# Optimization experiments

Measured on AMD Instinct MI355X. Metric: run time of the kernel, lower is better.

## Reference

```python
import jax, jax.numpy as jnp
import numpy as np

K = 3  # neighbors for knn_interpolate


def _knn_interpolate(x, pos, pos_skip, B, k):
    """PyG knn_interpolate with equal-sized batches.
    x: [N_coarse, C], pos: [N_coarse, 3], pos_skip: [N_fine, 3].
    """
    C = x.shape[1]
    xb = x.reshape(B, -1, C)          # [B, nc, C]
    pb = pos.reshape(B, -1, 3)        # [B, nc, 3]
    qb = pos_skip.reshape(B, -1, 3)   # [B, nf, 3]

    def per_cloud(xf, pf, qf):
        # squared distances [nf, nc]
        d2 = jnp.sum((qf[:, None, :] - pf[None, :, :]) ** 2, axis=-1)
        neg_d2k, idx = jax.lax.top_k(-d2, k)          # k smallest distances
        d2k = -neg_d2k                                # [nf, k]
        w = 1.0 / jnp.clip(d2k, 1e-16)                # inverse-distance weights
        w = jax.lax.stop_gradient(w)                  # PyG computes weights under no_grad
        feats = xf[idx]                               # [nf, k, C] gather
        return jnp.sum(w[..., None] * feats, axis=1) / jnp.sum(w, axis=1, keepdims=True)

    y = jax.vmap(per_cloud)(xb, pb, qb)               # [B, nf, C]
    return y.reshape(-1, C)


def setup_inputs() -> dict:
    key = jax.random.key(0)
    ks = jax.random.split(key, 8)
    B, n_coarse, n_fine = 16, 1024, 4096
    C_in, C_skip, C_mid, C_out = 256, 128, 256, 256
    x = jax.random.normal(ks[0], (B * n_coarse, C_in), jnp.float32)
    pos = jax.random.uniform(ks[1], (B * n_coarse, 3), jnp.float32)
    x_skip = jax.random.normal(ks[2], (B * n_fine, C_skip), jnp.float32)
    pos_skip = jax.random.uniform(ks[3], (B * n_fine, 3), jnp.float32)
    batch = jnp.repeat(jnp.arange(B, dtype=jnp.int64), n_coarse)
    batch_skip = jnp.repeat(jnp.arange(B, dtype=jnp.int64), n_fine)
    seed_idx = jnp.arange(B * n_coarse, dtype=jnp.int64)
    seed_idx_skip = jnp.arange(B * n_fine, dtype=jnp.int64)
    W1 = jax.random.normal(ks[4], (C_in + C_skip, C_mid), jnp.float32) * 0.05
    b1 = jnp.zeros((C_mid,), jnp.float32)
    W2 = jax.random.normal(ks[5], (C_mid, C_out), jnp.float32) * 0.05
    b2 = jnp.zeros((C_out,), jnp.float32)
    return {"x": x, "pos": pos, "batch": batch, "seed_idx": seed_idx,
            "x_skip": x_skip, "pos_skip": pos_skip, "batch_skip": batch_skip,
            "seed_idx_skip": seed_idx_skip, "W1": W1, "b1": b1, "W2": W2, "b2": b2}


def reference(x, pos, batch, seed_idx, x_skip, pos_skip, batch_skip, seed_idx_skip,
              W1, b1, W2, b2):
    B = int(batch[-1]) + 1  # equal-sized contiguous clouds
    y = _knn_interpolate(x, pos, pos_skip, B, K)      # [N_fine, C_in]
    h = jnp.concatenate([y, x_skip], axis=1)          # [N_fine, C_in+C_skip]
    h = jax.nn.relu(h @ W1 + b1)                      # MLP layer 1
    out = jax.nn.relu(h @ W2 + b2)                    # MLP layer 2
    return (out, pos_skip, batch_skip)
```

## Files before the change

kernel.cpp:

```cpp
#include <hip/hip_runtime.h>
#include <hip/hip_bf16.h>

#define NB    16
#define NC    1024
#define NF    4096
#define NFINE (NB*NF)
#define CIN   256
#define CSKIP 128
#define KH    (CIN+CSKIP)
#define CMID  256
#define COUT  256

typedef __attribute__((ext_vector_type(8))) short short8;
typedef __attribute__((ext_vector_type(4))) float f32x4;
typedef __attribute__((ext_vector_type(4))) unsigned int u32x4;

__device__ __forceinline__ float bf2f(short s) {
    return __uint_as_float(((unsigned)(unsigned short)s) << 16);
}

__global__ __launch_bounds__(256)
void binprep_kernel(const float* __restrict__ pos,
                    float* __restrict__ gp, int* __restrict__ gcs,
                    const float* __restrict__ W1, const float* __restrict__ W2,
                    __hip_bfloat16* __restrict__ W1at,
                    __hip_bfloat16* __restrict__ imgG,
                    __hip_bfloat16* __restrict__ img2)
{
    __shared__ int cnt[512];
    __shared__ float lx[NC], ly[NC], lz[NC];
    __shared__ short lcell[NC];
    const int t = threadIdx.x;
    if (blockIdx.x >= NB) {
        int e = (blockIdx.x - NB)*256 + t;
        if (e < CMID*CIN) {
            int n = e / CIN, k = e % CIN;
            W1at[e] = __float2bfloat16(W1[(size_t)k*CMID + n]);
        }
        int e2 = e - CMID*CIN;
        if (e2 >= 0 && e2 < 2*2048*8) {
            int chunk = e2 >> 3, el = e2 & 7;
            int s = chunk >> 11, L = chunk & 2047;
            int rr = L >> 3, sl = L & 7;
            int k = s*64 + ((sl ^ (rr & 7)) << 3) + el;
            imgG[e2] = __float2bfloat16(W1[(size_t)(CIN + k)*CMID + rr]);
        }
        int e3 = e2 - 2*2048*8;
        if (e3 >= 0 && e3 < 4*2048*8) {
            int chunk = e3 >> 3, el = e3 & 7;
            int s = chunk >> 11, L = chunk & 2047;
            int rr = L >> 3, sl = L & 7;
            int k = s*64 + ((sl ^ (rr & 7)) << 3) + el;
            img2[e3] = __float2bfloat16(W2[(size_t)k*COUT + rr]);
        }
        return;
    }
    const int b = blockIdx.x;
    for (int i = t; i < 512; i += 256) cnt[i] = 0;
    __syncthreads();
    const float* pc = pos + (size_t)b*NC*3;
    #pragma unroll
    for (int u = 0; u < 4; ++u) {
        int i = t + u*256;
        float x = pc[3*i+0], y = pc[3*i+1], z = pc[3*i+2];
        int cx = min(7, (int)(x*8.0f));
        int cy = min(7, (int)(y*8.0f));
        int cz = min(7, (int)(z*8.0f));
        int c = (cz*8 + cy)*8 + cx;
        lx[i] = x; ly[i] = y; lz[i] = z; lcell[i] = (short)c;
        atomicAdd(&cnt[c], 1);
    }
    __syncthreads();
    if (t < 64) {
        int v[8]; int s = 0;
        #pragma unroll
        for (int u = 0; u < 8; ++u) { v[u] = cnt[t*8+u]; s += v[u]; }
        int pfx = s;
        #pragma unroll
        for (int m = 1; m < 64; m <<= 1) {
            int o = __shfl_up(pfx, m);
            if (t >= m) pfx += o;
        }
        pfx -= s;
        #pragma unroll
        for (int u = 0; u < 8; ++u) {
            gcs[b*513 + t*8+u] = pfx;
            cnt[t*8+u] = pfx;
            pfx += v[u];
        }
        if (t == 63) gcs[b*513 + 512] = NC;
    }
    __syncthreads();
    #pragma unroll
    for (int u = 0; u < 4; ++u) {
        int i = t + u*256;
        int c = lcell[i];
        int dst = atomicAdd(&cnt[c], 1);
        f32x4 v; v[0] = lx[i]; v[1] = ly[i]; v[2] = lz[i]; v[3] = __int_as_float(i);
        *(f32x4*)&gp[(size_t)(b*NC + dst)*4] = v;
    }
}

#define KQPB 128

#define INS(d, j) do {                                        \
    bool c2 = (d) < dB, c1 = (d) < dA, c0 = (d) < d0;         \
    dB = c1 ? dA : (c2 ? (d) : dB);                           \
    iB = c1 ? iA : (c2 ? (j) : iB);                           \
    dA = c0 ? d0 : (c1 ? (d) : dA);                           \
    iA = c0 ? i0 : (c1 ? (j) : iA);                           \
    d0 = c0 ? (d) : d0;                                       \
    i0 = c0 ? (j) : i0;                                       \
} while (0)

#define SCAN(JS, JE) for (int j = (JS) + g; j < (JE); j += 4) {        \
    const f32x4 p = *(const f32x4*)&pp[j][0];                          \
    float fx = qx - p[0], fy = qy - p[1], fz = qz - p[2];              \
    float dd = fx*fx + fy*fy + fz*fz;                                  \
    INS(dd, j);                                                        \
}

#define MERGE4() do {                                                          \
    _Pragma("unroll")                                                          \
    for (int mm = 1; mm < 4; mm <<= 1) {                                       \
        float e0 = __shfl_xor(d0, mm), e1 = __shfl_xor(dA, mm), e2 = __shfl_xor(dB, mm); \
        int   f0 = __shfl_xor(i0, mm), f1 = __shfl_xor(iA, mm), f2 = __shfl_xor(iB, mm); \
        INS(e0, f0); INS(e1, f1); INS(e2, f2);                                 \
    }                                                                          \
} while (0)

union KZMem {
    struct { float pp[NC][4]; unsigned short cs[513]; } k;
    struct { short As[64][64]; short Bs[256][64]; } z;
};

__global__ __launch_bounds__(512, 2)
void knnZ_kernel(const float* __restrict__ pos_skip,
                 const float* __restrict__ gp,
                 const int* __restrict__ gcs,
                 int* __restrict__ widx, float* __restrict__ wval,
                 float* __restrict__ out,
                 const float* __restrict__ x,
                 const __hip_bfloat16* __restrict__ W1at,
                 __hip_bfloat16* __restrict__ Z)
{
    __shared__ __align__(16) KZMem sm;
    const int t = threadIdx.x;

    if (blockIdx.x >= 512) {
        const int m0 = (blockIdx.x - 512) * 64;
        const int wave = t >> 6, lane = t & 63;
        const int wm = wave >> 2, wn = wave & 3;
        const int rl = lane & 15, kq = lane >> 4;
        const short* Br = (const short*)W1at;
        const int ar = t >> 3;
        const int ac = t & 7;
        f32x4 rA[2];
        u32x4 rB[4];

        #define LOADAZ(K0) do {                                                \
            const float* p = &x[(size_t)(m0+ar)*CIN + (K0) + ac*8];            \
            rA[0] = *(const f32x4*)p; rA[1] = *(const f32x4*)(p+4);            \
        } while (0)
        #define LOADBZ(K0) do {                                                \
            _Pragma("unroll")                                                  \
            for (int i = 0; i < 4; ++i) {                                      \
                const int ch = t + i*512;                                      \
                const int rr = ch >> 3, cc = ch & 7;                           \
                rB[i] = *(const u32x4*)&Br[(size_t)rr*CIN + (K0) + cc*8];      \
            }                                                                  \
        } while (0)

        f32x4 acc[2][4] = {};
        LOADAZ(0); LOADBZ(0);
        #pragma unroll
        for (int s = 0; s < 4; ++s) {
            __syncthreads();
            {
                short8 sv;
                #pragma unroll
                for (int u = 0; u < 2; ++u) {
                    f32x4 a = rA[u];
                    #pragma unroll
                    for (int e = 0; e < 4; ++e) {
                        __hip_bfloat16 bb = __float2bfloat16(a[e]);
                        ((short*)&sv)[u*4+e] = *(short*)&bb;
                    }
                }
                *(short8*)&sm.z.As[ar][(ac ^ (ar&7))*8] = sv;
            }
            #pragma unroll
            for (int i = 0; i < 4; ++i) {
                const int ch = t + i*512;
                const int rr = ch >> 3, cc = ch & 7;
                *(u32x4*)&sm.z.Bs[rr][(cc ^ (rr&7))*8] = rB[i];
            }
            __syncthreads();
            if (s < 3) { LOADAZ((s+1)*64); LOADBZ((s+1)*64); }
            #pragma unroll
            for (int kh = 0; kh < 2; ++kh) {
                const int kc = kh*4 + kq;
                short8 af[2], bf[4];
                #pragma unroll
                for (int mf = 0; mf < 2; ++mf)
                    af[mf] = *(const short8*)&sm.z.As[wm*32 + mf*16 + rl][(kc ^ (rl&7))*8];
                #pragma unroll
                for (int nf = 0; nf < 4; ++nf)
                    bf[nf] = *(const short8*)&sm.z.Bs[wn*64 + nf*16 + rl][(kc ^ (rl&7))*8];
                #pragma unroll
                for (int mf = 0; mf < 2; ++mf)
                #pragma unroll
                for (int nf = 0; nf < 4; ++nf)
                    acc[mf][nf] = __builtin_amdgcn_mfma_f32_16x16x32_bf16(af[mf], bf[nf], acc[mf][nf], 0,0,0);
            }
        }
        #undef LOADAZ
        #undef LOADBZ
        #pragma unroll
        for (int mf = 0; mf < 2; ++mf)
        #pragma unroll
        for (int nf = 0; nf < 4; ++nf) {
            const int col = wn*64 + nf*16 + rl;
            #pragma unroll
            for (int i = 0; i < 4; ++i) {
                const int row = m0 + wm*32 + mf*16 + kq*4 + i;
                Z[(size_t)row*CMID + col] = __float2bfloat16(acc[mf][nf][i]);
            }
        }
        return;
    }

    float (*pp)[4] = sm.k.pp;
    unsigned short* cs = sm.k.cs;
    const int bpc = NF/KQPB;
    const int b  = blockIdx.x / bpc;
    const int qb = blockIdx.x % bpc;

    {
        if (t < 384) out[(size_t)NFINE*COUT + blockIdx.x*384 + t] = pos_skip[blockIdx.x*384 + t];
        if (t >= 384) {
            int e2 = blockIdx.x*128 + (t - 384);
            out[(size_t)NFINE*COUT + (size_t)NFINE*3 + e2] = (float)(e2 >> 12);
        }
    }

    for (int i = t; i < NC; i += 512)
        *(f32x4*)&pp[i][0] = *(const f32x4*)&gp[(size_t)(b*NC + i)*4];
    for (int i = t; i < 513; i += 512) cs[i] = (unsigned short)gcs[b*513 + i];
    __syncthreads();

    const int g  = t & 3;
    const int ql = t >> 2;
    const int q  = b*NF + qb*KQPB + ql;
    const float qx = pos_skip[(size_t)q*3+0];
    const float qy = pos_skip[(size_t)q*3+1];
    const float qz = pos_skip[(size_t)q*3+2];
    const int cx = min(7, (int)(qx*8.0f));
    const int cy = min(7, (int)(qy*8.0f));
    const int cz = min(7, (int)(qz*8.0f));

    float d0 = 3.0e38f, dA = 3.0e38f, dB = 3.0e38f;
    int   i0 = 0,       iA = 0,       iB = 0;

    const int xlo = max(cx-1,0), xhi = min(cx+1,7);
    const int ylo = max(cy-1,0), yhi = min(cy+1,7);
    const int zlo = max(cz-1,0), zhi = min(cz+1,7);
    #pragma unroll
    for (int r = 0; r < 9; ++r) {
        const int z = cz - 1 + r/3;
        const int y = cy - 1 + r%3;
        const bool ok = ((unsigned)z < 8u) & ((unsigned)y < 8u);
        const int rb = (z*8 + y)*8;
        int js = 0, je = 0;
        if (ok) { js = cs[rb + xlo]; je = cs[rb + xhi + 1]; }
        SCAN(js, je);
    }
    MERGE4();

    float m1 = 3.0e38f;
    if (xlo > 0) m1 = fminf(m1, qx - xlo*0.125f);
    if (xhi < 7) m1 = fminf(m1, (xhi+1)*0.125f - qx);
    if (ylo > 0) m1 = fminf(m1, qy - ylo*0.125f);
    if (yhi < 7) m1 = fminf(m1, (yhi+1)*0.125f - qy);
    if (zlo > 0) m1 = fminf(m1, qz - zlo*0.125f);
    if (zhi < 7) m1 = fminf(m1, (zhi+1)*0.125f - qz);

    if (dB > m1*m1) {
        const float s0 = d0, s1 = dA, s2 = dB;
        const int   t0 = i0, t1 = iA, t2 = iB;
        d0 = dA = dB = 3.0e38f; i0 = iA = iB = 0;
        const int xlo2 = max(cx-2,0), xhi2 = min(cx+2,7);
        const int ylo2 = max(cy-2,0), yhi2 = min(cy+2,7);
        const int zlo2 = max(cz-2,0), zhi2 = min(cz+2,7);
        for (int z = zlo2; z <= zhi2; ++z)
        for (int y = ylo2; y <= yhi2; ++y) {
            const int rb = (z*8 + y)*8;
            const bool inner_zy = (z >= zlo && z <= zhi && y >= ylo && y <= yhi);
            int jsA, jeA, jsB, jeB;
            if (inner_zy) {
                jsA = cs[rb + xlo2]; jeA = cs[rb + xlo];
                jsB = cs[rb + xhi + 1]; jeB = cs[rb + xhi2 + 1];
            } else {
                jsA = cs[rb + xlo2]; jeA = cs[rb + xhi2 + 1];
                jsB = 0; jeB = 0;
            }
            SCAN(jsA, jeA);
            SCAN(jsB, jeB);
        }
        MERGE4();
        INS(s0, t0); INS(s1, t1); INS(s2, t2);

        float m2 = 3.0e38f;
        if (xlo2 > 0) m2 = fminf(m2, qx - xlo2*0.125f);
        if (xhi2 < 7) m2 = fminf(m2, (xhi2+1)*0.125f - qx);
        if (ylo2 > 0) m2 = fminf(m2, qy - ylo2*0.125f);
        if (yhi2 < 7) m2 = fminf(m2, (yhi2+1)*0.125f - qy);
        if (zlo2 > 0) m2 = fminf(m2, qz - zlo2*0.125f);
        if (zhi2 < 7) m2 = fminf(m2, (zhi2+1)*0.125f - qz);
        if (dB > m2*m2) {
            const float u0 = d0, u1 = dA, u2 = dB;
            const int   v0 = i0, v1 = iA, v2 = iB;
            d0 = dA = dB = 3.0e38f; i0 = iA = iB = 0;
            for (int j = g; j < NC; j += 4) {
                const f32x4 p = *(const f32x4*)&pp[j][0];
                int pcx = min(7, (int)(p[0]*8.0f));
                int pcy = min(7, (int)(p[1]*8.0f));
                int pcz = min(7, (int)(p[2]*8.0f));
                if (pcx >= xlo2 && pcx <= xhi2 && pcy >= ylo2 && pcy <= yhi2 &&
                    pcz >= zlo2 && pcz <= zhi2) continue;
                float fx = qx - p[0], fy = qy - p[1], fz = qz - p[2];
                float dd = fx*fx + fy*fy + fz*fz;
                INS(dd, j);
            }
            MERGE4();
            INS(u0, v0); INS(u1, v1); INS(u2, v2);
        }
    }

    if (g == 0) {
        const int o0 = __float_as_int(pp[i0][3]);
        const int o1 = __float_as_int(pp[iA][3]);
        const int o2 = __float_as_int(pp[iB][3]);
        float w0 = 1.0f / fmaxf(d0, 1e-16f);
        float w1 = 1.0f / fmaxf(dA, 1e-16f);
        float w2 = 1.0f / fmaxf(dB, 1e-16f);
        float inv = 1.0f / (w0 + w1 + w2);
        widx[q*3+0] = b*NC + o0;  wval[q*3+0] = w0*inv;
        widx[q*3+1] = b*NC + o1;  wval[q*3+1] = w1*inv;
        widx[q*3+2] = b*NC + o2;  wval[q*3+2] = w2*inv;
    }
}

__global__ __launch_bounds__(512, 2)
void g2_fused(const float* __restrict__ x_skip,
              const float* __restrict__ b1,
              const __hip_bfloat16* __restrict__ Z,
              const int* __restrict__ widx,
              const float* __restrict__ wval,
              const __hip_bfloat16* __restrict__ imgG,
              const __hip_bfloat16* __restrict__ img2,
              const float* __restrict__ b2,
              float* __restrict__ out)
{
    __shared__ __align__(16) short As[64][128];
    __shared__ __align__(16) short Bs[256][64];
    __shared__ __align__(16) short Hs[64][256];
    const int nwg = gridDim.x;
    const int tile = (blockIdx.x & 7)*(nwg >> 3) + (blockIdx.x >> 3);
    const int m0 = tile * 64;

    const int t = threadIdx.x;
    const int wave = t >> 6, lane = t & 63;
    const int wm = wave >> 2, wn = wave & 3;
    const int rl = lane & 15, kq = lane >> 4;
    const short* gI = (const short*)imgG;
    const short* g2i = (const short*)img2;
    const short* Zr  = (const short*)Z;
    short* BsLin = &Bs[0][0];
    short (*BsH)[64] = (short(*)[64])&Hs[0][0];

    const int ar = t >> 3;
    const int ac = t & 7;

    const float* xs = &x_skip[(size_t)(m0+ar)*CSKIP];
    f32x4 pa0 = *(const f32x4*)&xs[ac*8];
    f32x4 pa1 = *(const f32x4*)&xs[ac*8+4];
    f32x4 pb0 = *(const f32x4*)&xs[64+ac*8];
    f32x4 pb1 = *(const f32x4*)&xs[64+ac*8+4];
    u32x4 rG0[4], rG1[4];
    #pragma unroll
    for (int i = 0; i < 4; ++i) {
        rG0[i] = *(const u32x4*)&gI[(size_t)(       i*512 + t)*8];
        rG1[i] = *(const u32x4*)&gI[(size_t)(2048 + i*512 + t)*8];
    }

    {
        short8 sv0, sv1;
        #pragma unroll
        for (int u = 0; u < 2; ++u) {
            f32x4 a = (u == 0) ? pa0 : pa1;
            f32x4 b = (u == 0) ? pb0 : pb1;
            #pragma unroll
            for (int e = 0; e < 4; ++e) {
                __hip_bfloat16 ba = __float2bfloat16(a[e]);
                __hip_bfloat16 bb = __float2bfloat16(b[e]);
                ((short*)&sv0)[u*4+e] = *(short*)&ba;
                ((short*)&sv1)[u*4+e] = *(short*)&bb;
            }
        }
        const int sw = ac ^ (ar & 7);
        *(short8*)&As[ar][sw*8]     = sv0;
        *(short8*)&As[ar][(8+sw)*8] = sv1;
    }
    #pragma unroll
    for (int i = 0; i < 4; ++i) {
        *(u32x4*)&BsLin[(size_t)(i*512 + t)*8]       = rG0[i];
        *(u32x4*)&(&Hs[0][0])[(size_t)(i*512 + t)*8] = rG1[i];
    }
    __syncthreads();

    f32x4 acc[2][4] = {};
    #pragma unroll
    for (int kh = 0; kh < 2; ++kh) {
        const int kc = kh*4 + kq;
        short8 af[2], bf[4];
        #pragma unroll
        for (int mf = 0; mf < 2; ++mf)
            af[mf] = *(const short8*)&As[wm*32 + mf*16 + rl][((kc ^ (rl&7)))*8];
        #pragma unroll
        for (int nf = 0; nf < 4; ++nf)
            bf[nf] = *(const short8*)&Bs[wn*64 + nf*16 + rl][(kc ^ (rl&7))*8];
        #pragma unroll
        for (int mf = 0; mf < 2; ++mf)
        #pragma unroll
        for (int nf = 0; nf < 4; ++nf)
            acc[mf][nf] = __builtin_amdgcn_mfma_f32_16x16x32_bf16(af[mf], bf[nf], acc[mf][nf], 0,0,0);
    }
    #pragma unroll
    for (int kh = 0; kh < 2; ++kh) {
        const int kc = kh*4 + kq;
        short8 af[2], bf[4];
        #pragma unroll
        for (int mf = 0; mf < 2; ++mf)
            af[mf] = *(const short8*)&As[wm*32 + mf*16 + rl][(8 + (kc ^ (rl&7)))*8];
        #pragma unroll
        for (int nf = 0; nf < 4; ++nf)
            bf[nf] = *(const short8*)&BsH[wn*64 + nf*16 + rl][(kc ^ (rl&7))*8];
        #pragma unroll
        for (int mf = 0; mf < 2; ++mf)
        #pragma unroll
        for (int nf = 0; nf < 4; ++nf)
            acc[mf][nf] = __builtin_amdgcn_mfma_f32_16x16x32_bf16(af[mf], bf[nf], acc[mf][nf], 0,0,0);
    }
    __syncthreads();

    u32x4 rB[4];
    #pragma unroll
    for (int i = 0; i < 4; ++i)
        rB[i] = *(const u32x4*)&g2i[(size_t)(i*512 + t)*8];
    #pragma unroll
    for (int mf = 0; mf < 2; ++mf)
    #pragma unroll
    for (int nf = 0; nf < 4; ++nf) {
        const int col = wn*64 + nf*16 + rl;
        const float bv = b1[col];
        #pragma unroll
        for (int i = 0; i < 4; ++i) {
            const int row = wm*32 + mf*16 + kq*4 + i;
            float v = acc[mf][nf][i] + bv;
            __hip_bfloat16 bb = __float2bfloat16(v);
            Hs[row][((col >> 3) ^ (row & 7))*8 + (col & 7)] = *(short*)&bb;
        }
    }
    #pragma unroll
    for (int i = 0; i < 4; ++i)
        *(u32x4*)&BsLin[(size_t)(i*512 + t)*8] = rB[i];
    __syncthreads();

    #pragma unroll
    for (int u = 0; u < 4; ++u) {
        const int ch = t + u*512;
        const int row = ch >> 5;
        const int cc  = ch & 31;
        const int c   = cc * 8;
        const int gr = (m0 + row)*3;
        const int j0 = widx[gr+0], j1 = widx[gr+1], j2 = widx[gr+2];
        const float w0 = wval[gr+0], w1 = wval[gr+1], w2 = wval[gr+2];
        const short8 z0 = *(const short8*)&Zr[(size_t)j0*CMID + c];
        const short8 z1 = *(const short8*)&Zr[(size_t)j1*CMID + c];
        const short8 z2 = *(const short8*)&Zr[(size_t)j2*CMID + c];
        const int slot = (cc ^ (row & 7))*8;
        short8 gchunk = *(const short8*)&Hs[row][slot];
        short8 r;
        #pragma unroll
        for (int e = 0; e < 8; ++e) {
            float v = bf2f(gchunk[e]) + w0*bf2f(z0[e]) + w1*bf2f(z1[e]) + w2*bf2f(z2[e]);
            v = fmaxf(v, 0.0f);
            __hip_bfloat16 bb = __float2bfloat16(v);
            r[e] = *(short*)&bb;
        }
        *(short8*)&Hs[row][slot] = r;
    }
    __syncthreads();

    f32x4 acc2[2][4] = {};
    #define MFMA2(S2) do {                                                     \
        _Pragma("unroll")                                                      \
        for (int kh = 0; kh < 2; ++kh) {                                       \
            const int kcl = kh*4 + kq;                                         \
            const int kca = (S2)*8 + kcl;                                      \
            short8 af[2], bf[4];                                               \
            _Pragma("unroll")                                                  \
            for (int mf = 0; mf < 2; ++mf)                                     \
                af[mf] = *(const short8*)&Hs[wm*32 + mf*16 + rl][(kca ^ (rl&7))*8]; \
            _Pragma("unroll")                                                  \
            for (int nf = 0; nf < 4; ++nf)                                     \
                bf[nf] = *(const short8*)&Bs[wn*64 + nf*16 + rl][(kcl ^ (rl&7))*8]; \
            _Pragma("unroll")                                                  \
            for (int mf = 0; mf < 2; ++mf)                                     \
            _Pragma("unroll")                                                  \
            for (int nf = 0; nf < 4; ++nf)                                     \
                acc2[mf][nf] = __builtin_amdgcn_mfma_f32_16x16x32_bf16(af[mf], bf[nf], acc2[mf][nf], 0,0,0); \
        }                                                                      \
    } while (0)
    #define LOADI2(S) do {                                                     \
        _Pragma("unroll")                                                      \
        for (int i = 0; i < 4; ++i)                                            \
            rB[i] = *(const u32x4*)&g2i[(size_t)((S)*2048 + i*512 + t)*8];     \
    } while (0)
    #define STAGEI2() do {                                                     \
        _Pragma("unroll")                                                      \
        for (int i = 0; i < 4; ++i)                                            \
            *(u32x4*)&BsLin[(size_t)(i*512 + t)*8] = rB[i];                    \
    } while (0)

    LOADI2(1);
    MFMA2(0);
    __syncthreads();
    STAGEI2();
    __syncthreads();
    LOADI2(2);
    MFMA2(1);
    __syncthreads();
    STAGEI2();
    __syncthreads();
    LOADI2(3);
    MFMA2(2);
    __syncthreads();
    STAGEI2();
    __syncthreads();
    MFMA2(3);

    #pragma unroll
    for (int mf = 0; mf < 2; ++mf)
    #pragma unroll
    for (int nf = 0; nf < 4; ++nf) {
        const int col = wn*64 + nf*16 + rl;
        const float bv = b2[col];
        #pragma unroll
        for (int i = 0; i < 4; ++i) {
            const int row = m0 + wm*32 + mf*16 + kq*4 + i;
            out[(size_t)row*COUT + col] = fmaxf(acc2[mf][nf][i] + bv, 0.0f);
        }
    }
    #undef MFMA2
    #undef LOADI2
    #undef STAGEI2
}

extern "C" void kernel_launch(void* const* d_in, const int* in_sizes, int n_in,
                              void* d_out, int out_size, void* d_ws, size_t ws_size,
                              hipStream_t stream) {
    const float* x        = (const float*)d_in[0];
    const float* pos      = (const float*)d_in[1];
    const float* x_skip   = (const float*)d_in[4];
    const float* pos_skip = (const float*)d_in[5];
    const float* W1       = (const float*)d_in[8];
    const float* b1       = (const float*)d_in[9];
    const float* W2       = (const float*)d_in[10];
    const float* b2       = (const float*)d_in[11];
    float* out = (float*)d_out;
    char* ws = (char*)d_ws;

    int*            widx = (int*)  (ws + 0);
    float*          wval = (float*)(ws + 786432);
    __hip_bfloat16* W1at = (__hip_bfloat16*)(ws + 1572864);
    __hip_bfloat16* imgG = (__hip_bfloat16*)(ws + 1703936);
    __hip_bfloat16* img2 = (__hip_bfloat16*)(ws + 1769472);
    float*          gp   = (float*)(ws + 1900544);
    int*            gcs  = (int*)  (ws + 2162688);
    __hip_bfloat16* Z    = (__hip_bfloat16*)(ws + 2195520);

    hipLaunchKernelGGL(binprep_kernel, dim3(NB + 640), dim3(256), 0, stream,
                       pos, gp, gcs, W1, W2, W1at, imgG, img2);
    hipLaunchKernelGGL(knnZ_kernel, dim3(512 + 256), dim3(512), 0, stream,
                       pos_skip, gp, gcs, widx, wval, out, x, W1at, Z);
    hipLaunchKernelGGL(g2_fused, dim3(NFINE/64), dim3(512), 0, stream,
                       x_skip, b1, Z, widx, wval, imgG, img2, b2, out);
}
```

Before: 64.27 us.

## Process two 64-row tiles per workgroup in g2_fused with prefetched x_skip

Each g2_fused workgroup now handles two consecutive 64-row tiles in a loop, and the grid is halved to 512 blocks. The second tile's x_skip rows are prefetched into registers while the first tile is computed, and the imgG weight registers are reused across both tiles. Output stores become nontemporal. This amortises per-block startup and weight loads, but gives fewer blocks (512 on a 256-CU device at 2 blocks/CU, about one wave of blocks) and a longer serial chain per block.

```diff
diff --git a/kernel.cpp b/kernel.cpp
--- a/kernel.cpp
+++ b/kernel.cpp
@@ -366,8 +366,7 @@
     __shared__ __align__(16) short Bs[256][64];
     __shared__ __align__(16) short Hs[64][256];
     const int nwg = gridDim.x;
-    const int tile = (blockIdx.x & 7)*(nwg >> 3) + (blockIdx.x >> 3);
-    const int m0 = tile * 64;
+    const int pair = (blockIdx.x & 7)*(nwg >> 3) + (blockIdx.x >> 3);
 
     const int t = threadIdx.x;
     const int wave = t >> 6, lane = t & 63;
@@ -381,12 +380,8 @@
 
     const int ar = t >> 3;
     const int ac = t & 7;
-
-    const float* xs = &x_skip[(size_t)(m0+ar)*CSKIP];
-    f32x4 pa0 = *(const f32x4*)&xs[ac*8];
-    f32x4 pa1 = *(const f32x4*)&xs[ac*8+4];
-    f32x4 pb0 = *(const f32x4*)&xs[64+ac*8];
-    f32x4 pb1 = *(const f32x4*)&xs[64+ac*8+4];
+    const int sw = ac ^ (ar & 7);
+
     u32x4 rG0[4], rG1[4];
     #pragma unroll
     for (int i = 0; i < 4; ++i) {
@@ -394,178 +389,202 @@
         rG1[i] = *(const u32x4*)&gI[(size_t)(2048 + i*512 + t)*8];
     }
 
+    int m0 = pair * 128;
+    f32x4 pa0, pa1, pb0, pb1;
     {
-        short8 sv0, sv1;
-        #pragma unroll
-        for (int u = 0; u < 2; ++u) {
-            f32x4 a = (u == 0) ? pa0 : pa1;
-            f32x4 b = (u == 0) ? pb0 : pb1;
-            #pragma unroll
-            for (int e = 0; e < 4; ++e) {
-                __hip_bfloat16 ba = __float2bfloat16(a[e]);
-                __hip_bfloat16 bb = __float2bfloat16(b[e]);
-                ((short*)&sv0)[u*4+e] = *(short*)&ba;
-                ((short*)&sv1)[u*4+e] = *(short*)&bb;
-            }
-        }
-        const int sw = ac ^ (ar & 7);
-        *(short8*)&As[ar][sw*8]     = sv0;
-        *(short8*)&As[ar][(8+sw)*8] = sv1;
-    }
-    #pragma unroll
-    for (int i = 0; i < 4; ++i) {
-        *(u32x4*)&BsLin[(size_t)(i*512 + t)*8]       = rG0[i];
-        *(u32x4*)&(&Hs[0][0])[(size_t)(i*512 + t)*8] = rG1[i];
-    }
-    __syncthreads();
-
-    f32x4 acc[2][4] = {};
-    #pragma unroll
-    for (int kh = 0; kh < 2; ++kh) {
-        const int kc = kh*4 + kq;
-        short8 af[2], bf[4];
+        const float* xs = &x_skip[(size_t)(m0+ar)*CSKIP];
+        pa0 = *(const f32x4*)&xs[ac*8];
+        pa1 = *(const f32x4*)&xs[ac*8+4];
+        pb0 = *(const f32x4*)&xs[64+ac*8];
+        pb1 = *(const f32x4*)&xs[64+ac*8+4];
+    }
+
+    for (int half = 0; half < 2; ++half) {
+        {
+            short8 sv0, sv1;
+            #pragma unroll
+            for (int u = 0; u < 2; ++u) {
+                f32x4 a = (u == 0) ? pa0 : pa1;
+                f32x4 b = (u == 0) ? pb0 : pb1;
+                #pragma unroll
+                for (int e = 0; e < 4; ++e) {
+                    __hip_bfloat16 ba = __float2bfloat16(a[e]);
+                    __hip_bfloat16 bb = __float2bfloat16(b[e]);
+                    ((short*)&sv0)[u*4+e] = *(short*)&ba;
+                    ((short*)&sv1)[u*4+e] = *(short*)&bb;
+                }
+            }
+            *(short8*)&As[ar][sw*8]     = sv0;
+            *(short8*)&As[ar][(8+sw)*8] = sv1;
+        }
+        #pragma unroll
+        for (int i = 0; i < 4; ++i) {
+            *(u32x4*)&BsLin[(size_t)(i*512 + t)*8]       = rG0[i];
+            *(u32x4*)&(&Hs[0][0])[(size_t)(i*512 + t)*8] = rG1[i];
+        }
+        if (half == 0) {
+            const float* xs2 = &x_skip[(size_t)(m0+64+ar)*CSKIP];
+            pa0 = *(const f32x4*)&xs2[ac*8];
+            pa1 = *(const f32x4*)&xs2[ac*8+4];
+            pb0 = *(const f32x4*)&xs2[64+ac*8];
+            pb1 = *(const f32x4*)&xs2[64+ac*8+4];
+        }
+        __syncthreads();
+
+        f32x4 acc[2][4] = {};
+        #pragma unroll
+        for (int kh = 0; kh < 2; ++kh) {
+            const int kc = kh*4 + kq;
+            short8 af[2], bf[4];
+            #pragma unroll
+            for (int mf = 0; mf < 2; ++mf)
+                af[mf] = *(const short8*)&As[wm*32 + mf*16 + rl][((kc ^ (rl&7)))*8];
+            #pragma unroll
+            for (int nf = 0; nf < 4; ++nf)
+                bf[nf] = *(const short8*)&Bs[wn*64 + nf*16 + rl][(kc ^ (rl&7))*8];
+            #pragma unroll
+            for (int mf = 0; mf < 2; ++mf)
+            #pragma unroll
+            for (int nf = 0; nf < 4; ++nf)
+                acc[mf][nf] = __builtin_amdgcn_mfma_f32_16x16x32_bf16(af[mf], bf[nf], acc[mf][nf], 0,0,0);
+        }
+        #pragma unroll
+        for (int kh = 0; kh < 2; ++kh) {
+            const int kc = kh*4 + kq;
+            short8 af[2], bf[4];
+            #pragma unroll
+            for (int mf = 0; mf < 2; ++mf)
+                af[mf] = *(const short8*)&As[wm*32 + mf*16 + rl][(8 + (kc ^ (rl&7)))*8];
+            #pragma unroll
+            for (int nf = 0; nf < 4; ++nf)
+                bf[nf] = *(const short8*)&BsH[wn*64 + nf*16 + rl][(kc ^ (rl&7))*8];
+            #pragma unroll
+            for (int mf = 0; mf < 2; ++mf)
+            #pragma unroll
+            for (int nf = 0; nf < 4; ++nf)
+                acc[mf][nf] = __builtin_amdgcn_mfma_f32_16x16x32_bf16(af[mf], bf[nf], acc[mf][nf], 0,0,0);
+        }
+        __syncthreads();
+
+        u32x4 rB[4];
+        #pragma unroll
+        for (int i = 0; i < 4; ++i)
+            rB[i] = *(const u32x4*)&g2i[(size_t)(i*512 + t)*8];
         #pragma unroll
         for (int mf = 0; mf < 2; ++mf)
-            af[mf] = *(const short8*)&As[wm*32 + mf*16 + rl][((kc ^ (rl&7)))*8];
-        #pragma unroll
-        for (int nf = 0; nf < 4; ++nf)
-            bf[nf] = *(const short8*)&Bs[wn*64 + nf*16 + rl][(kc ^ (rl&7))*8];
+        #pragma unroll
+        for (int nf = 0; nf < 4; ++nf) {
+            const int col = wn*64 + nf*16 + rl;
+            const float bv = b1[col];
+            #pragma unroll
+            for (int i = 0; i < 4; ++i) {
+                const int row = wm*32 + mf*16 + kq*4 + i;
+                float v = acc[mf][nf][i] + bv;
+                __hip_bfloat16 bb = __float2bfloat16(v);
+                Hs[row][((col >> 3) ^ (row & 7))*8 + (col & 7)] = *(short*)&bb;
+            }
+        }
+        #pragma unroll
+        for (int i = 0; i < 4; ++i)
+            *(u32x4*)&BsLin[(size_t)(i*512 + t)*8] = rB[i];
+        __syncthreads();
+
+        #pragma unroll
+        for (int u = 0; u < 4; ++u) {
+            const int ch = t + u*512;
+            const int row = ch >> 5;
+            const int cc  = ch & 31;
+            const int c   = cc * 8;
+            const int gr = (m0 + row)*3;
+            const int j0 = widx[gr+0], j1 = widx[gr+1], j2 = widx[gr+2];
+            const float w0 = wval[gr+0], w1 = wval[gr+1], w2 = wval[gr+2];
+            const short8 z0 = *(const short8*)&Zr[(size_t)j0*CMID + c];
+            const short8 z1 = *(const short8*)&Zr[(size_t)j1*CMID + c];
+            const short8 z2 = *(const short8*)&Zr[(size_t)j2*CMID + c];
+            const int slot = (cc ^ (row & 7))*8;
+            short8 gchunk = *(const short8*)&Hs[row][slot];
+            short8 r;
+            #pragma unroll
+            for (int e = 0; e < 8; ++e) {
+                float v = bf2f(gchunk[e]) + w0*bf2f(z0[e]) + w1*bf2f(z1[e]) + w2*bf2f(z2[e]);
+                v = fmaxf(v, 0.0f);
+                __hip_bfloat16 bb = __float2bfloat16(v);
+                r[e] = *(short*)&bb;
+            }
+            *(short8*)&Hs[row][slot] = r;
+        }
+        __syncthreads();
+
+        f32x4 acc2[2][4] = {};
+        #define MFMA2(S2) do {                                                     \
+            _Pragma("unroll")                                                      \
+            for (int kh = 0; kh < 2; ++kh) {                                       \
+                const int kcl = kh*4 + kq;                                         \
+                const int kca = (S2)*8 + kcl;                                      \
+                short8 af[2], bf[4];                                               \
+                _Pragma("unroll")                                                  \
+                for (int mf = 0; mf < 2; ++mf)                                     \
+                    af[mf] = *(const short8*)&Hs[wm*32 + mf*16 + rl][(kca ^ (rl&7))*8]; \
+                _Pragma("unroll")                                                  \
+                for (int nf = 0; nf < 4; ++nf)                                     \
+                    bf[nf] = *(const short8*)&Bs[wn*64 + nf*16 + rl][(kcl ^ (rl&7))*8]; \
+                _Pragma("unroll")                                                  \
+                for (int mf = 0; mf < 2; ++mf)                                     \
+                _Pragma("unroll")                                                  \
+                for (int nf = 0; nf < 4; ++nf)                                     \
+                    acc2[mf][nf] = __builtin_amdgcn_mfma_f32_16x16x32_bf16(af[mf], bf[nf], acc2[mf][nf], 0,0,0); \
+            }                                                                      \
+        } while (0)
+        #define LOADI2(S) do {                                                     \
+            _Pragma("unroll")                                                      \
+            for (int i = 0; i < 4; ++i)                                            \
+                rB[i] = *(const u32x4*)&g2i[(size_t)((S)*2048 + i*512 + t)*8];     \
+        } while (0)
+        #define STAGEI2() do {                                                     \
+            _Pragma("unroll")                                                      \
+            for (int i = 0; i < 4; ++i)                                            \
+                *(u32x4*)&BsLin[(size_t)(i*512 + t)*8] = rB[i];                    \
+        } while (0)
+
+        LOADI2(1);
+        MFMA2(0);
+        __syncthreads();
+        STAGEI2();
+        __syncthreads();
+        LOADI2(2);
+        MFMA2(1);
+        __syncthreads();
+        STAGEI2();
+        __syncthreads();
+        LOADI2(3);
+        MFMA2(2);
+        __syncthreads();
+        STAGEI2();
+        __syncthreads();
+        MFMA2(3);
+        #undef MFMA2
+        #undef LOADI2
+        #undef STAGEI2
+
         #pragma unroll
         for (int mf = 0; mf < 2; ++mf)
         #pragma unroll
-        for (int nf = 0; nf < 4; ++nf)
-            acc[mf][nf] = __builtin_amdgcn_mfma_f32_16x16x32_bf16(af[mf], bf[nf], acc[mf][nf], 0,0,0);
-    }
-    #pragma unroll
-    for (int kh = 0; kh < 2; ++kh) {
-        const int kc = kh*4 + kq;
-        short8 af[2], bf[4];
-        #pragma unroll
-        for (int mf = 0; mf < 2; ++mf)
-            af[mf] = *(const short8*)&As[wm*32 + mf*16 + rl][(8 + (kc ^ (rl&7)))*8];
-        #pragma unroll
-        for (int nf = 0; nf < 4; ++nf)
-            bf[nf] = *(const short8*)&BsH[wn*64 + nf*16 + rl][(kc ^ (rl&7))*8];
-        #pragma unroll
-        for (int mf = 0; mf < 2; ++mf)
-        #pragma unroll
-        for (int nf = 0; nf < 4; ++nf)
-            acc[mf][nf] = __builtin_amdgcn_mfma_f32_16x16x32_bf16(af[mf], bf[nf], acc[mf][nf], 0,0,0);
-    }
-    __syncthreads();
-
-    u32x4 rB[4];
-    #pragma unroll
-    for (int i = 0; i < 4; ++i)
-        rB[i] = *(const u32x4*)&g2i[(size_t)(i*512 + t)*8];
-    #pragma unroll
-    for (int mf = 0; mf < 2; ++mf)
-    #pragma unroll
-    for (int nf = 0; nf < 4; ++nf) {
-        const int col = wn*64 + nf*16 + rl;
-        const float bv = b1[col];
-        #pragma unroll
-        for (int i = 0; i < 4; ++i) {
-            const int row = wm*32 + mf*16 + kq*4 + i;
-            float v = acc[mf][nf][i] + bv;
-            __hip_bfloat16 bb = __float2bfloat16(v);
-            Hs[row][((col >> 3) ^ (row & 7))*8 + (col & 7)] = *(short*)&bb;
-        }
-    }
-    #pragma unroll
-    for (int i = 0; i < 4; ++i)
-        *(u32x4*)&BsLin[(size_t)(i*512 + t)*8] = rB[i];
-    __syncthreads();
-
-    #pragma unroll
-    for (int u = 0; u < 4; ++u) {
-        const int ch = t + u*512;
-        const int row = ch >> 5;
-        const int cc  = ch & 31;
-        const int c   = cc * 8;
-        const int gr = (m0 + row)*3;
-        const int j0 = widx[gr+0], j1 = widx[gr+1], j2 = widx[gr+2];
-        const float w0 = wval[gr+0], w1 = wval[gr+1], w2 = wval[gr+2];
-        const short8 z0 = *(const short8*)&Zr[(size_t)j0*CMID + c];
-        const short8 z1 = *(const short8*)&Zr[(size_t)j1*CMID + c];
-        const short8 z2 = *(const short8*)&Zr[(size_t)j2*CMID + c];
-        const int slot = (cc ^ (row & 7))*8;
-        short8 gchunk = *(const short8*)&Hs[row][slot];
-        short8 r;
-        #pragma unroll
-        for (int e = 0; e < 8; ++e) {
-            float v = bf2f(gchunk[e]) + w0*bf2f(z0[e]) + w1*bf2f(z1[e]) + w2*bf2f(z2[e]);
-            v = fmaxf(v, 0.0f);
-            __hip_bfloat16 bb = __float2bfloat16(v);
-            r[e] = *(short*)&bb;
-        }
-        *(short8*)&Hs[row][slot] = r;
-    }
-    __syncthreads();
-
-    f32x4 acc2[2][4] = {};
-    #define MFMA2(S2) do {                                                     \
-        _Pragma("unroll")                                                      \
-        for (int kh = 0; kh < 2; ++kh) {                                       \
-            const int kcl = kh*4 + kq;                                         \
-            const int kca = (S2)*8 + kcl;                                      \
-            short8 af[2], bf[4];                                               \
-            _Pragma("unroll")                                                  \
-            for (int mf = 0; mf < 2; ++mf)                                     \
-                af[mf] = *(const short8*)&Hs[wm*32 + mf*16 + rl][(kca ^ (rl&7))*8]; \
-            _Pragma("unroll")                                                  \
-            for (int nf = 0; nf < 4; ++nf)                                     \
-                bf[nf] = *(const short8*)&Bs[wn*64 + nf*16 + rl][(kcl ^ (rl&7))*8]; \
-            _Pragma("unroll")                                                  \
-            for (int mf = 0; mf < 2; ++mf)                                     \
-            _Pragma("unroll")                                                  \
-            for (int nf = 0; nf < 4; ++nf)                                     \
-                acc2[mf][nf] = __builtin_amdgcn_mfma_f32_16x16x32_bf16(af[mf], bf[nf], acc2[mf][nf], 0,0,0); \
-        }                                                                      \
-    } while (0)
-    #define LOADI2(S) do {                                                     \
-        _Pragma("unroll")                                                      \
-        for (int i = 0; i < 4; ++i)                                            \
-            rB[i] = *(const u32x4*)&g2i[(size_t)((S)*2048 + i*512 + t)*8];     \
-    } while (0)
-    #define STAGEI2() do {                                                     \
-        _Pragma("unroll")                                                      \
-        for (int i = 0; i < 4; ++i)                                            \
-            *(u32x4*)&BsLin[(size_t)(i*512 + t)*8] = rB[i];                    \
-    } while (0)
-
-    LOADI2(1);
-    MFMA2(0);
-    __syncthreads();
-    STAGEI2();
-    __syncthreads();
-    LOADI2(2);
-    MFMA2(1);
-    __syncthreads();
-    STAGEI2();
-    __syncthreads();
-    LOADI2(3);
-    MFMA2(2);
-    __syncthreads();
-    STAGEI2();
-    __syncthreads();
-    MFMA2(3);
-
-    #pragma unroll
-    for (int mf = 0; mf < 2; ++mf)
-    #pragma unroll
-    for (int nf = 0; nf < 4; ++nf) {
-        const int col = wn*64 + nf*16 + rl;
-        const float bv = b2[col];
-        #pragma unroll
-        for (int i = 0; i < 4; ++i) {
-            const int row = m0 + wm*32 + mf*16 + kq*4 + i;
-            out[(size_t)row*COUT + col] = fmaxf(acc2[mf][nf][i] + bv, 0.0f);
-        }
-    }
-    #undef MFMA2
-    #undef LOADI2
-    #undef STAGEI2
+        for (int nf = 0; nf < 4; ++nf) {
+            const int col = wn*64 + nf*16 + rl;
+            const float bv = b2[col];
+            #pragma unroll
+            for (int i = 0; i < 4; ++i) {
+                const int row = m0 + wm*32 + mf*16 + kq*4 + i;
+                __builtin_nontemporal_store(fmaxf(acc2[mf][nf][i] + bv, 0.0f),
+                                            &out[(size_t)row*COUT + col]);
+            }
+        }
+
+        if (half == 0) {
+            m0 += 64;
+            __syncthreads();
+        }
+    }
 }
 
 extern "C" void kernel_launch(void* const* d_in, const int* in_sizes, int n_in,
@@ -595,6 +614,6 @@
                        pos, gp, gcs, W1, W2, W1at, imgG, img2);
     hipLaunchKernelGGL(knnZ_kernel, dim3(512 + 256), dim3(512), 0, stream,
                        pos_skip, gp, gcs, widx, wval, out, x, W1at, Z);
-    hipLaunchKernelGGL(g2_fused, dim3(NFINE/64), dim3(512), 0, stream,
+    hipLaunchKernelGGL(g2_fused, dim3(NFINE/128), dim3(512), 0, stream,
                        x_skip, b1, Z, widx, wval, imgG, img2, b2, out);
 }
```

Result: slower. 71.93 us (+11.9%).
